# Kernel tuning notes

Hardware: AMD Instinct MI355X
Metric: run time of the kernel (lower is better)

Reference implementation:

```python
import jax, jax.numpy as jnp
import numpy as np
from jax import lax

LR, SB, LB = 256, 16, 8  # lr_size, spatial_bin, luma_bins
DN = ('NCHW', 'OIHW', 'NCHW')


def conv2d(x, w, b=None, stride=1, pad=1):
    out = lax.conv_general_dilated(x, w, (stride, stride), [(pad, pad), (pad, pad)], dimension_numbers=DN)
    return out if b is None else out + b[None, :, None, None]


def gaussian_blur17(x):
    # kornia GaussianBlur2d(kernel=(17,17), sigma=(2,2)), reflect padding, separable
    t = jnp.arange(17, dtype=x.dtype) - 8.0
    g = jnp.exp(-(t * t) / 8.0)  # 2*sigma^2 = 8
    g = g / g.sum()
    C = x.shape[1]
    xp = jnp.pad(x, ((0, 0), (0, 0), (8, 8), (8, 8)), mode='reflect')
    kh = jnp.broadcast_to(g.reshape(1, 1, 17, 1), (C, 1, 17, 1))
    kw = jnp.broadcast_to(g.reshape(1, 1, 1, 17), (C, 1, 1, 17))
    x1 = lax.conv_general_dilated(xp, kh, (1, 1), 'VALID', dimension_numbers=DN, feature_group_count=C)
    return lax.conv_general_dilated(x1, kw, (1, 1), 'VALID', dimension_numbers=DN, feature_group_count=C)


def nearest_resize(x, size):
    # torch F.interpolate mode='nearest': src = floor(dst * in/out)
    H, W = x.shape[-2], x.shape[-1]
    iy = jnp.floor(jnp.arange(size) * (H / size)).astype(jnp.int32)
    ix = jnp.floor(jnp.arange(size) * (W / size)).astype(jnp.int32)
    return x[:, :, iy][:, :, :, ix]


def grid_sample_3d_border(inp, grid):
    # inp [B,C,D,Hi,Wi]; grid [B,Do,Ho,Wo,3] with (x,y,z); bilinear, padding_mode='border', align_corners=False
    B, C, D, Hi, Wi = inp.shape
    x = jnp.clip(((grid[..., 0] + 1.0) * Wi - 1.0) * 0.5, 0.0, Wi - 1.0)
    y = jnp.clip(((grid[..., 1] + 1.0) * Hi - 1.0) * 0.5, 0.0, Hi - 1.0)
    z = jnp.clip(((grid[..., 2] + 1.0) * D - 1.0) * 0.5, 0.0, D - 1.0)
    x0 = jnp.floor(x); y0 = jnp.floor(y); z0 = jnp.floor(z)
    fx = (x - x0)[:, None]; fy = (y - y0)[:, None]; fz = (z - z0)[:, None]  # [B,1,Do,Ho,Wo]
    x0i = x0.astype(jnp.int32); y0i = y0.astype(jnp.int32); z0i = z0.astype(jnp.int32)
    x1i = jnp.minimum(x0i + 1, Wi - 1); y1i = jnp.minimum(y0i + 1, Hi - 1); z1i = jnp.minimum(z0i + 1, D - 1)
    flat = inp.reshape(B, C, D * Hi * Wi)
    M = grid.shape[1] * grid.shape[2] * grid.shape[3]

    def gat(zi, yi, xi):
        idx = ((zi * Hi + yi) * Wi + xi).reshape(B, 1, M)
        v = jnp.take_along_axis(flat, jnp.broadcast_to(idx, (B, C, M)), axis=2)
        return v.reshape(B, C, grid.shape[1], grid.shape[2], grid.shape[3])

    return (gat(z0i, y0i, x0i) * (1 - fz) * (1 - fy) * (1 - fx)
            + gat(z0i, y0i, x1i) * (1 - fz) * (1 - fy) * fx
            + gat(z0i, y1i, x0i) * (1 - fz) * fy * (1 - fx)
            + gat(z0i, y1i, x1i) * (1 - fz) * fy * fx
            + gat(z1i, y0i, x0i) * fz * (1 - fy) * (1 - fx)
            + gat(z1i, y0i, x1i) * fz * (1 - fy) * fx
            + gat(z1i, y1i, x0i) * fz * fy * (1 - fx)
            + gat(z1i, y1i, x1i) * fz * fy * fx)


def _forward(lqs, evs, gw1, gb1, gw2, gb2, sw0, sb0, sw1, sb1, sw2, sb2, sw3, sb3,
             cw0, cb0, cw1, cb1, fw1, fb1, fw2, fb2, fw3, fb3, lw1, lb1, lw2, fuw, fub):
    B, _, H, W = lqs.shape
    # --- HighresStreamNet guide ---
    g = gaussian_blur17(lqs)
    g = jax.nn.relu(conv2d(g, gw1, gb1, 1, 0))
    guide = jax.nn.sigmoid(conv2d(g, gw2, gb2, 1, 0)) * 2.0 - 0.5  # [B,1,H,W]
    # --- slicing grid (x,y in (-0.5,1.5) per source, z = guide) ---
    gx = (jnp.arange(W, dtype=lqs.dtype) + 0.5) / W * 2.0 - 0.5
    gy = (jnp.arange(H, dtype=lqs.dtype) + 0.5) / H * 2.0 - 0.5
    gyy, gxx = jnp.meshgrid(gy, gx, indexing='ij')
    base = jnp.broadcast_to(jnp.stack([gxx, gyy], -1)[None, None], (B, 1, H, W, 2))
    grid = jnp.concatenate([base, guide[..., None]], axis=-1)  # [B,1,H,W,3]
    # --- LowresStreamNet ---
    lr = nearest_resize(lqs, LR)
    ev = evs if (evs.shape[-1] == LR and evs.shape[-2] == LR) else nearest_resize(evs, LR)
    x = jnp.concatenate([lr, ev], axis=1)  # [B,18,256,256]
    for w_, b_ in ((sw0, sb0), (sw1, sb1), (sw2, sb2), (sw3, sb3)):
        x = jax.nn.relu(conv2d(x, w_, b_, 2, 1))  # -> [B,64,16,16]
    xl = conv2d(jax.nn.relu(conv2d(x, lw1, lb1, 1, 1)), lw2, None, 1, 1)  # local, last conv no bias
    xg = jax.nn.relu(conv2d(x, cw0, cb0, 2, 1))
    xg = jax.nn.relu(conv2d(xg, cw1, cb1, 2, 1)).reshape(B, -1)  # [B,1024]
    xg = jax.nn.relu(xg @ fw1.T + fb1)
    xg = jax.nn.relu(xg @ fw2.T + fb2)
    xg = xg @ fw3.T + fb3  # [B,64]
    fused = jax.nn.relu(xg[:, :, None, None] + xl)
    bg = conv2d(fused, fuw, fub, 1, 0).reshape(B, 1, LB, SB, SB)  # bilateral grid [B,1,8,16,16]
    hr = grid_sample_3d_border(bg, grid)  # [B,1,1,H,W]
    return hr.reshape(B, -1, H, W)


def setup_inputs():
    key = jax.random.key(0)
    ks = iter(jax.random.split(key, 40))

    def W_(shape):
        fan_in = int(np.prod(shape[1:]))
        return jax.random.normal(next(ks), shape, jnp.float32) * np.float32(np.sqrt(2.0 / fan_in))

    def Z(n):
        return jnp.zeros((n,), jnp.float32)

    B, H, Wd = 8, 1024, 1024
    return {
        'lqs': jax.random.uniform(next(ks), (B, 3, H, Wd), jnp.float32),
        'evs': jax.random.normal(next(ks), (B, 15, 256, 256), jnp.float32) * 0.1,
        'gw1': W_((16, 3, 1, 1)), 'gb1': Z(16), 'gw2': W_((1, 16, 1, 1)), 'gb2': Z(1),
        'sw0': W_((8, 18, 3, 3)), 'sb0': Z(8), 'sw1': W_((16, 8, 3, 3)), 'sb1': Z(16),
        'sw2': W_((32, 16, 3, 3)), 'sb2': Z(32), 'sw3': W_((64, 32, 3, 3)), 'sb3': Z(64),
        'cw0': W_((64, 64, 3, 3)), 'cb0': Z(64), 'cw1': W_((64, 64, 3, 3)), 'cb1': Z(64),
        'fw1': W_((256, 1024)), 'fb1': Z(256), 'fw2': W_((128, 256)), 'fb2': Z(128),
        'fw3': W_((64, 128)), 'fb3': Z(64),
        'lw1': W_((64, 64, 3, 3)), 'lb1': Z(64), 'lw2': W_((64, 64, 3, 3)),
        'fuw': W_((8, 64, 1, 1)), 'fub': Z(8),
    }


def reference(lqs, evs, gw1, gb1, gw2, gb2, sw0, sb0, sw1, sb1, sw2, sb2, sw3, sb3,
              cw0, cb0, cw1, cb1, fw1, fb1, fw2, fb2, fw3, fb3, lw1, lb1, lw2, fuw, fub):
    return _forward(lqs, evs, gw1, gb1, gw2, gb2, sw0, sb0, sw1, sb1, sw2, sb2, sw3, sb3,
                    cw0, cb0, cw1, cb1, fw1, fb1, fw2, fb2, fw3, fb3, lw1, lb1, lw2, fuw, fub)
```

## Files before the change

kernel.cpp:

```cpp
#include <hip/hip_runtime.h>
#include <hip/hip_bf16.h>
#include <math.h>

#define BATCH 8
#define HH 1024
#define WW 1024

__device__ __forceinline__ int reflect1024(int i) {
    i = i < 0 ? -i : i;
    return i > 1023 ? 2046 - i : i;
}

__global__ __launch_bounds__(256) void conv0_k(const float* __restrict__ lqs,
                                               const float* __restrict__ evs,
                                               const float* __restrict__ w,
                                               const float* __restrict__ bias,
                                               float* __restrict__ out) {
    int idx = blockIdx.x * 256 + threadIdx.x;
    int q = idx & 4095;
    int b = idx >> 12;
    int qx = q & 31, oy = q >> 5;
    int iy0 = oy * 2 - 1;

    float acc[4][8];
#pragma unroll
    for (int j = 0; j < 4; ++j)
#pragma unroll
        for (int o = 0; o < 8; ++o) acc[j][o] = bias[o];

#pragma unroll
    for (int ic = 0; ic < 3; ++ic) {
        const float* ipc = lqs + (size_t)(b * 3 + ic) * HH * WW;
#pragma unroll
        for (int ky = 0; ky < 3; ++ky) {
            int iy = iy0 + ky;
            if (iy < 0) continue;
            const float* row = ipc + (size_t)iy * 4 * WW;
            float xr[9];
#pragma unroll
            for (int i = 0; i < 9; ++i) {
                int ix = 8 * qx - 1 + i;
                xr[i] = (ix >= 0) ? row[ix * 4] : 0.0f;
            }
#pragma unroll
            for (int o = 0; o < 8; ++o) {
                const float* wp = w + (o * 18 + ic) * 9 + ky * 3;
#pragma unroll
                for (int j = 0; j < 4; ++j)
#pragma unroll
                    for (int kx = 0; kx < 3; ++kx)
                        acc[j][o] = fmaf(wp[kx], xr[2 * j + kx], acc[j][o]);
            }
        }
    }
    for (int ic = 0; ic < 15; ++ic) {
        const float* ipc = evs + (size_t)(b * 15 + ic) * 65536;
#pragma unroll
        for (int ky = 0; ky < 3; ++ky) {
            int iy = iy0 + ky;
            if (iy < 0) continue;
            const float* row = ipc + iy * 256;
            const float4* r4 = (const float4*)row;
            float4 A = r4[2 * qx];
            float4 Bv = r4[2 * qx + 1];
            float m = (qx > 0) ? row[8 * qx - 1] : 0.0f;
            float xr[9] = {m, A.x, A.y, A.z, A.w, Bv.x, Bv.y, Bv.z, Bv.w};
#pragma unroll
            for (int o = 0; o < 8; ++o) {
                const float* wp = w + (o * 18 + ic + 3) * 9 + ky * 3;
#pragma unroll
                for (int j = 0; j < 4; ++j)
#pragma unroll
                    for (int kx = 0; kx < 3; ++kx)
                        acc[j][o] = fmaf(wp[kx], xr[2 * j + kx], acc[j][o]);
            }
        }
    }
#pragma unroll
    for (int o = 0; o < 8; ++o) {
        float4 v = make_float4(fmaxf(acc[0][o], 0.0f), fmaxf(acc[1][o], 0.0f),
                               fmaxf(acc[2][o], 0.0f), fmaxf(acc[3][o], 0.0f));
        *(float4*)(out + ((size_t)(b * 8 + o) << 14) + oy * 128 + qx * 4) = v;
    }
}

template <int IC, int OC, int OCT, int IH, int IW, int STRIDE, bool RELU, bool HASB>
__global__ __launch_bounds__(256) void convN_k(const float* __restrict__ in,
                                               const float* __restrict__ w,
                                               const float* __restrict__ bias,
                                               float* __restrict__ out) {
    constexpr int OH = (IH + 2 - 3) / STRIDE + 1;
    constexpr int OW = (IW + 2 - 3) / STRIDE + 1;
    constexpr int POS = OH * OW;
    constexpr int G = OC / OCT;
    int idx = blockIdx.x * 256 + threadIdx.x;
    if (idx >= BATCH * G * POS) return;
    int px = idx % POS;
    int g = (idx / POS) % G;
    int b = idx / (POS * G);
    int ox = px % OW, oy = px / OW;
    int iy0 = oy * STRIDE - 1, ix0 = ox * STRIDE - 1;

    float acc[OCT];
#pragma unroll
    for (int o = 0; o < OCT; ++o) acc[o] = HASB ? bias[g * OCT + o] : 0.0f;

    const float* ip = in + (size_t)b * IC * IH * IW;
    for (int ic = 0; ic < IC; ++ic) {
        const float* ipc = ip + ic * IH * IW;
        float x[9];
#pragma unroll
        for (int ky = 0; ky < 3; ++ky) {
            int iy = iy0 + ky;
#pragma unroll
            for (int kx = 0; kx < 3; ++kx) {
                int ix = ix0 + kx;
                bool ok = (iy >= 0) && (iy < IH) && (ix >= 0) && (ix < IW);
                x[ky * 3 + kx] = ok ? ipc[iy * IW + ix] : 0.0f;
            }
        }
#pragma unroll
        for (int o = 0; o < OCT; ++o) {
            const float* wp = w + ((g * OCT + o) * IC + ic) * 9;
#pragma unroll
            for (int k = 0; k < 9; ++k) acc[o] = fmaf(wp[k], x[k], acc[o]);
        }
    }
#pragma unroll
    for (int o = 0; o < OCT; ++o) {
        float v = acc[o];
        if (RELU) v = fmaxf(v, 0.0f);
        out[(size_t)(b * OC + g * OCT + o) * POS + px] = v;
    }
}

template <int IC, int OC, int OCT, int IH, int IW, int STRIDE, int SPLIT>
__global__ __launch_bounds__(256) void convS_k(const float* __restrict__ in,
                                               const float* __restrict__ w,
                                               float* __restrict__ part) {
    constexpr int OH = (IH + 2 - 3) / STRIDE + 1;
    constexpr int OW = (IW + 2 - 3) / STRIDE + 1;
    constexpr int POS = OH * OW;
    constexpr int G = OC / OCT;
    constexpr int TOT = BATCH * G * POS;
    constexpr int ICS = IC / SPLIT;
    constexpr int N = BATCH * OC * POS;
    int idx = blockIdx.x * 256 + threadIdx.x;
    if (idx >= TOT * SPLIT) return;
    int s = idx / TOT, r = idx % TOT;
    int px = r % POS;
    int g = (r / POS) % G;
    int b = r / (POS * G);
    int ox = px % OW, oy = px / OW;
    int iy0 = oy * STRIDE - 1, ix0 = ox * STRIDE - 1;

    float acc[OCT];
#pragma unroll
    for (int o = 0; o < OCT; ++o) acc[o] = 0.0f;

    const float* ip = in + (size_t)b * IC * IH * IW;
    for (int ic = s * ICS; ic < (s + 1) * ICS; ++ic) {
        const float* ipc = ip + ic * IH * IW;
        float x[9];
#pragma unroll
        for (int ky = 0; ky < 3; ++ky) {
            int iy = iy0 + ky;
#pragma unroll
            for (int kx = 0; kx < 3; ++kx) {
                int ix = ix0 + kx;
                bool ok = (iy >= 0) && (iy < IH) && (ix >= 0) && (ix < IW);
                x[ky * 3 + kx] = ok ? ipc[iy * IW + ix] : 0.0f;
            }
        }
#pragma unroll
        for (int o = 0; o < OCT; ++o) {
            const float* wp = w + ((g * OCT + o) * IC + ic) * 9;
#pragma unroll
            for (int k = 0; k < 9; ++k) acc[o] = fmaf(wp[k], x[k], acc[o]);
        }
    }
#pragma unroll
    for (int o = 0; o < OCT; ++o)
        part[(size_t)s * N + (size_t)(b * OC + g * OCT + o) * POS + px] = acc[o];
}

__global__ __launch_bounds__(256) void fc1_k(const float* __restrict__ part_cw1,
                                             const float* __restrict__ cb1,
                                             const float* __restrict__ fw1,
                                             const float* __restrict__ fb1,
                                             float* __restrict__ h1) {
    __shared__ float xin[1024];
    int t = threadIdx.x;
    int b = blockIdx.x >> 6;
    int rgrp = blockIdx.x & 63;
    int wave = t >> 6, lane = t & 63;

    for (int i = t; i < 1024; i += 256) {
        float v = cb1[i >> 4];
#pragma unroll
        for (int s = 0; s < 16; ++s) v += part_cw1[s * 8192 + b * 1024 + i];
        xin[i] = fmaxf(v, 0.0f);
    }
    __syncthreads();

    int r = (rgrp << 2) | wave;
    const float4* w4 = (const float4*)(fw1 + r * 1024);
    const float4* x4 = (const float4*)xin;
    float acc = 0.0f;
#pragma unroll
    for (int jj = 0; jj < 4; ++jj) {
        float4 wv = w4[lane + 64 * jj];
        float4 xv = x4[lane + 64 * jj];
        acc = fmaf(wv.x, xv.x, acc);
        acc = fmaf(wv.y, xv.y, acc);
        acc = fmaf(wv.z, xv.z, acc);
        acc = fmaf(wv.w, xv.w, acc);
    }
#pragma unroll
    for (int m = 32; m; m >>= 1) acc += __shfl_xor(acc, m, 64);
    if (lane == 0) h1[b * 256 + r] = fmaxf(acc + fb1[r], 0.0f);
}

__global__ __launch_bounds__(256) void fc23fuse_k(const float* __restrict__ h1,
                                                  const float* __restrict__ fw2,
                                                  const float* __restrict__ fb2,
                                                  const float* __restrict__ fw3,
                                                  const float* __restrict__ fb3,
                                                  const float* __restrict__ xl2,
                                                  const float* __restrict__ fuw,
                                                  const float* __restrict__ fub,
                                                  float* __restrict__ bg) {
    __shared__ float h2[128];
    __shared__ float xg[64];
    int b = blockIdx.x, t = threadIdx.x;
    int wave = t >> 6, lane = t & 63;

    float4 xv1 = ((const float4*)(h1 + b * 256))[lane];
#pragma unroll 4
    for (int i = 0; i < 32; ++i) {
        int r = wave * 32 + i;
        float4 wv = ((const float4*)(fw2 + r * 256))[lane];
        float acc = fmaf(wv.x, xv1.x, fmaf(wv.y, xv1.y, fmaf(wv.z, xv1.z, wv.w * xv1.w)));
#pragma unroll
        for (int m = 32; m; m >>= 1) acc += __shfl_xor(acc, m, 64);
        if (lane == 0) h2[r] = fmaxf(acc + fb2[r], 0.0f);
    }
    __syncthreads();

    float2 xv2 = ((const float2*)h2)[lane];
#pragma unroll 4
    for (int i = 0; i < 16; ++i) {
        int r = wave * 16 + i;
        float2 wv = ((const float2*)(fw3 + r * 128))[lane];
        float acc = fmaf(wv.x, xv2.x, wv.y * xv2.y);
#pragma unroll
        for (int m = 32; m; m >>= 1) acc += __shfl_xor(acc, m, 64);
        if (lane == 0) xg[r] = acc + fb3[r];
    }
    __syncthreads();

    int px = t;
    float acc[8];
#pragma unroll
    for (int d = 0; d < 8; ++d) acc[d] = fub[d];
    for (int c = 0; c < 64; ++c) {
        float f = fmaxf(xg[c] + xl2[(b * 64 + c) * 256 + px], 0.0f);
#pragma unroll
        for (int d = 0; d < 8; ++d) acc[d] = fmaf(fuw[d * 64 + c], f, acc[d]);
    }
#pragma unroll
    for (int d = 0; d < 8; ++d) bg[(b * 8 + d) * 256 + px] = acc[d];
}

__global__ __launch_bounds__(256) void guide_slice_k(const float* __restrict__ lqs,
                                                     const float* __restrict__ bgp,
                                                     const float* __restrict__ gw1,
                                                     const float* __restrict__ gb1,
                                                     const float* __restrict__ gw2,
                                                     const float* __restrict__ gb2,
                                                     float* __restrict__ out) {
    constexpr int TW = 64, TH = 32;
    __shared__ float sBH[3][TH][81];
    __shared__ float sBG[2048];
    __shared__ float sW1[48], sB1[16], sW2[16], sB2v[1];

    int t = threadIdx.x;
    int bx = blockIdx.x & 15;
    int by = (blockIdx.x >> 4) & 31;
    int b = blockIdx.x >> 9;
    int x0 = bx * TW, y0 = by * TH;

    float gv[17];
    {
        float gs = 0.0f;
#pragma unroll
        for (int i = 0; i < 17; ++i) {
            float d = (float)i - 8.0f;
            gv[i] = expf(-(d * d) * 0.125f);
            gs += gv[i];
        }
        float inv = 1.0f / gs;
#pragma unroll
        for (int i = 0; i < 17; ++i) gv[i] *= inv;
    }

    for (int i = t; i < 2048; i += 256) sBG[i] = bgp[b * 2048 + i];
    if (t < 48) sW1[t] = gw1[t];
    if (t < 16) { sB1[t] = gb1[t]; sW2[t] = gw2[t]; }
    if (t == 0) sB2v[0] = gb2[0];

    if (t < 240) {
        int c = t / 80, xo = t % 80;
        int gx = reflect1024(x0 + xo - 8);
        const float* colp = lqs + (size_t)(b * 3 + c) * HH * WW + gx;
        float win[17];
#pragma unroll
        for (int i = 0; i < 16; ++i)
            win[i] = colp[(size_t)reflect1024(y0 - 8 + i) * WW];
#pragma unroll
        for (int j = 0; j < TH; ++j) {
            win[(16 + j) % 17] = colp[(size_t)reflect1024(y0 + 8 + j) * WW];
            float acc = 0.0f;
#pragma unroll
            for (int i = 0; i < 17; ++i) acc = fmaf(gv[i], win[(j + i) % 17], acc);
            sBH[c][j][xo] = acc;
        }
    }
    __syncthreads();

    int yy = t >> 3, xs = (t & 7) * 8;
    int Y = y0 + yy;
    float fy = fminf(fmaxf((Y + 0.5f) * (1.0f / 64.0f) + 3.5f, 0.0f), 15.0f);
    float yf = floorf(fy);
    int yi = (int)yf;
    float ay = fy - yf;
    int yi1 = min(yi + 1, 15);

    float bcv[3][8];
#pragma unroll
    for (int c = 0; c < 3; ++c) {
        float win[17];
#pragma unroll
        for (int i = 0; i < 16; ++i) win[i] = sBH[c][yy][xs + i];
#pragma unroll
        for (int j = 0; j < 8; ++j) {
            win[(16 + j) % 17] = sBH[c][yy][xs + 16 + j];
            float acc = 0.0f;
#pragma unroll
            for (int i = 0; i < 17; ++i) acc = fmaf(gv[i], win[(j + i) % 17], acc);
            bcv[c][j] = acc;
        }
    }

    float val[8];
#pragma unroll
    for (int j = 0; j < 8; ++j) {
        float b0 = bcv[0][j], b1 = bcv[1][j], b2 = bcv[2][j];
        float s = sB2v[0];
#pragma unroll
        for (int c = 0; c < 16; ++c) {
            float g1 = fmaf(sW1[c * 3 + 0], b0,
                       fmaf(sW1[c * 3 + 1], b1,
                       fmaf(sW1[c * 3 + 2], b2, sB1[c])));
            s = fmaf(sW2[c], fmaxf(g1, 0.0f), s);
        }
        float sig = 1.0f / (1.0f + expf(-s));
        float guide = sig * 2.0f - 0.5f;

        int X = x0 + xs + j;
        float fx = fminf(fmaxf((X + 0.5f) * (1.0f / 64.0f) + 3.5f, 0.0f), 15.0f);
        float fz = fminf(fmaxf(fmaf(guide, 4.0f, 3.5f), 0.0f), 7.0f);
        float xf = floorf(fx), zf = floorf(fz);
        int xi = (int)xf, zi = (int)zf;
        float ax = fx - xf, az = fz - zf;
        int xi1 = min(xi + 1, 15), zi1 = min(zi + 1, 7);

        const float* g0 = sBG + zi * 256;
        const float* g1p = sBG + zi1 * 256;
        int i00 = yi * 16 + xi, i01 = yi * 16 + xi1;
        int i10 = yi1 * 16 + xi, i11 = yi1 * 16 + xi1;
        float c00 = g0[i00] + az * (g1p[i00] - g0[i00]);
        float c01 = g0[i01] + az * (g1p[i01] - g0[i01]);
        float c10 = g0[i10] + az * (g1p[i10] - g0[i10]);
        float c11 = g0[i11] + az * (g1p[i11] - g0[i11]);
        float c0 = c00 + ay * (c10 - c00);
        float c1 = c01 + ay * (c11 - c01);
        val[j] = c0 + ax * (c1 - c0);
    }
    float4* op = (float4*)(out + (size_t)b * HH * WW + (size_t)Y * WW + x0 + xs);
    op[0] = make_float4(val[0], val[1], val[2], val[3]);
    op[1] = make_float4(val[4], val[5], val[6], val[7]);
}

extern "C" void kernel_launch(void* const* d_in, const int* in_sizes, int n_in,
                              void* d_out, int out_size, void* d_ws, size_t ws_size,
                              hipStream_t stream) {
    const float* lqs = (const float*)d_in[0];
    const float* evs = (const float*)d_in[1];
    const float* gw1 = (const float*)d_in[2];
    const float* gb1 = (const float*)d_in[3];
    const float* gw2 = (const float*)d_in[4];
    const float* gb2 = (const float*)d_in[5];
    const float* sw0 = (const float*)d_in[6];
    const float* sb0 = (const float*)d_in[7];
    const float* sw1 = (const float*)d_in[8];
    const float* sb1 = (const float*)d_in[9];
    const float* sw2 = (const float*)d_in[10];
    const float* sb2 = (const float*)d_in[11];
    const float* sw3 = (const float*)d_in[12];
    const float* sb3 = (const float*)d_in[13];
    const float* cw0 = (const float*)d_in[14];
    const float* cb0 = (const float*)d_in[15];
    const float* cw1 = (const float*)d_in[16];
    const float* cb1 = (const float*)d_in[17];
    const float* fw1 = (const float*)d_in[18];
    const float* fb1 = (const float*)d_in[19];
    const float* fw2 = (const float*)d_in[20];
    const float* fb2 = (const float*)d_in[21];
    const float* fw3 = (const float*)d_in[22];
    const float* fb3 = (const float*)d_in[23];
    const float* lw1 = (const float*)d_in[24];
    const float* lb1 = (const float*)d_in[25];
    const float* lw2 = (const float*)d_in[26];
    const float* fuw = (const float*)d_in[27];
    const float* fub = (const float*)d_in[28];
    float* out = (float*)d_out;

    float* ws = (float*)d_ws;
    float* o0 = ws;
    float* o1 = o0 + 1048576;
    float* o2 = o1 + 524288;
    float* o3 = o2 + 262144;
    float* xl1 = o3 + 131072;
    float* xl2 = xl1 + 131072;
    float* xg0 = xl2 + 131072;
    float* h1 = xg0 + 32768;
    float* bg = h1 + 2048;
    float* part_cw1 = bg + 16384;

    conv0_k<<<128, 256, 0, stream>>>(lqs, evs, sw0, sb0, o0);
    convN_k<8, 16, 4, 128, 128, 2, true, true><<<512, 256, 0, stream>>>(o0, sw1, sb1, o1);
    convN_k<16, 32, 2, 64, 64, 2, true, true><<<512, 256, 0, stream>>>(o1, sw2, sb2, o2);
    convN_k<32, 64, 1, 32, 32, 2, true, true><<<512, 256, 0, stream>>>(o2, sw3, sb3, o3);
    convN_k<64, 64, 1, 16, 16, 1, true, true><<<512, 256, 0, stream>>>(o3, lw1, lb1, xl1);
    convN_k<64, 64, 1, 16, 16, 1, false, false><<<512, 256, 0, stream>>>(xl1, lw2, nullptr, xl2);
    convN_k<64, 64, 1, 16, 16, 2, true, true><<<128, 256, 0, stream>>>(o3, cw0, cb0, xg0);
    convS_k<64, 64, 4, 8, 8, 2, 16><<<128, 256, 0, stream>>>(xg0, cw1, part_cw1);
    fc1_k<<<512, 256, 0, stream>>>(part_cw1, cb1, fw1, fb1, h1);
    fc23fuse_k<<<8, 256, 0, stream>>>(h1, fw2, fb2, fw3, fb3, xl2, fuw, fub, bg);
    guide_slice_k<<<BATCH * 32 * 16, 256, 0, stream>>>(lqs, bg, gw1, gb1, gw2, gb2, out);
}
```

Baseline: 485.1 us.

## Split conv input channels across blocks with partial-sum reduce kernels

Replaces the direct convolution kernels for the low-resolution splat and local layers with split-K style convS kernels. Each one writes per-split partial sums that a small reduce kernel then combines, adding bias and ReLU. The lw2 partials are summed directly inside the fuse kernel, which removes one reduce pass. The aim is more parallelism for these small, deep-channel convs, at the cost of extra launches and partial-buffer memory traffic. The first conv's output-channel tiling parameter is also changed.

After: 431.2 us. 1.13x faster.

```diff
diff --git a/kernel.cpp b/kernel.cpp
--- a/kernel.cpp
+++ b/kernel.cpp
@@ -184,6 +184,20 @@
         part[(size_t)s * N + (size_t)(b * OC + g * OCT + o) * POS + px] = acc[o];
 }
 
+template <int OC, int POS, int SPLIT, bool RELU, bool HASB>
+__global__ __launch_bounds__(256) void reduce_k(const float* __restrict__ part,
+                                                const float* __restrict__ bias,
+                                                float* __restrict__ out) {
+    constexpr int N = BATCH * OC * POS;
+    int idx = blockIdx.x * 256 + threadIdx.x;
+    if (idx >= N) return;
+    int oc = (idx / POS) % OC;
+    float a = HASB ? bias[oc] : 0.0f;
+#pragma unroll
+    for (int s = 0; s < SPLIT; ++s) a += part[(size_t)s * N + idx];
+    out[idx] = RELU ? fmaxf(a, 0.0f) : a;
+}
+
 __global__ __launch_bounds__(256) void fc1_k(const float* __restrict__ part_cw1,
                                              const float* __restrict__ cb1,
                                              const float* __restrict__ fw1,
@@ -226,7 +240,7 @@
                                                   const float* __restrict__ fb2,
                                                   const float* __restrict__ fw3,
                                                   const float* __restrict__ fb3,
-                                                  const float* __restrict__ xl2,
+                                                  const float* __restrict__ part_lw2,
                                                   const float* __restrict__ fuw,
                                                   const float* __restrict__ fub,
                                                   float* __restrict__ bg) {
@@ -264,7 +278,11 @@
 #pragma unroll
     for (int d = 0; d < 8; ++d) acc[d] = fub[d];
     for (int c = 0; c < 64; ++c) {
-        float f = fmaxf(xg[c] + xl2[(b * 64 + c) * 256 + px], 0.0f);
+        int base = (b * 64 + c) * 256 + px;
+        float xlv = 0.0f;
+#pragma unroll
+        for (int s = 0; s < 8; ++s) xlv += part_lw2[s * 131072 + base];
+        float f = fmaxf(xg[c] + xlv, 0.0f);
 #pragma unroll
         for (int d = 0; d < 8; ++d) acc[d] = fmaf(fuw[d * 64 + c], f, acc[d]);
     }
@@ -432,21 +450,26 @@
     float* o2 = o1 + 524288;
     float* o3 = o2 + 262144;
     float* xl1 = o3 + 131072;
-    float* xl2 = xl1 + 131072;
-    float* xg0 = xl2 + 131072;
+    float* xg0 = xl1 + 131072;
     float* h1 = xg0 + 32768;
     float* bg = h1 + 2048;
-    float* part_cw1 = bg + 16384;
+    float* partA = bg + 16384;
+    float* part_lw2 = partA + 1048576;
+    float* part_cw1 = part_lw2 + 1048576;
 
     conv0_k<<<128, 256, 0, stream>>>(lqs, evs, sw0, sb0, o0);
-    convN_k<8, 16, 4, 128, 128, 2, true, true><<<512, 256, 0, stream>>>(o0, sw1, sb1, o1);
-    convN_k<16, 32, 2, 64, 64, 2, true, true><<<512, 256, 0, stream>>>(o1, sw2, sb2, o2);
-    convN_k<32, 64, 1, 32, 32, 2, true, true><<<512, 256, 0, stream>>>(o2, sw3, sb3, o3);
-    convN_k<64, 64, 1, 16, 16, 1, true, true><<<512, 256, 0, stream>>>(o3, lw1, lb1, xl1);
-    convN_k<64, 64, 1, 16, 16, 1, false, false><<<512, 256, 0, stream>>>(xl1, lw2, nullptr, xl2);
-    convN_k<64, 64, 1, 16, 16, 2, true, true><<<128, 256, 0, stream>>>(o3, cw0, cb0, xg0);
+    convN_k<8, 16, 8, 128, 128, 2, true, true><<<256, 256, 0, stream>>>(o0, sw1, sb1, o1);
+    convS_k<16, 32, 8, 64, 64, 2, 4><<<512, 256, 0, stream>>>(o1, sw2, partA);
+    reduce_k<32, 1024, 4, true, true><<<1024, 256, 0, stream>>>(partA, sb2, o2);
+    convS_k<32, 64, 8, 32, 32, 2, 8><<<512, 256, 0, stream>>>(o2, sw3, partA);
+    reduce_k<64, 256, 8, true, true><<<512, 256, 0, stream>>>(partA, sb3, o3);
+    convS_k<64, 64, 8, 16, 16, 1, 8><<<512, 256, 0, stream>>>(o3, lw1, partA);
+    reduce_k<64, 256, 8, true, true><<<512, 256, 0, stream>>>(partA, lb1, xl1);
+    convS_k<64, 64, 8, 16, 16, 1, 8><<<512, 256, 0, stream>>>(xl1, lw2, part_lw2);
+    convS_k<64, 64, 8, 16, 16, 2, 16><<<256, 256, 0, stream>>>(o3, cw0, partA);
+    reduce_k<64, 64, 16, true, true><<<128, 256, 0, stream>>>(partA, cb0, xg0);
     convS_k<64, 64, 4, 8, 8, 2, 16><<<128, 256, 0, stream>>>(xg0, cw1, part_cw1);
     fc1_k<<<512, 256, 0, stream>>>(part_cw1, cb1, fw1, fb1, h1);
-    fc23fuse_k<<<8, 256, 0, stream>>>(h1, fw2, fb2, fw3, fb3, xl2, fuw, fub, bg);
+    fc23fuse_k<<<8, 256, 0, stream>>>(h1, fw2, fb2, fw3, fb3, part_lw2, fuw, fub, bg);
     guide_slice_k<<<BATCH * 32 * 16, 256, 0, stream>>>(lqs, bg, gw1, gb1, gw2, gb2, out);
 }
```

## Overlap guide blur with low-res conv chain via heterogeneous fused launches

Applied to the files above, without the earlier changes.

Splits the full-resolution blur and guide MLP out of the final slice kernel and distributes its 4096 tiles across the six small conv launches. Those launches run conv blocks and blur blocks side by side, so otherwise idle compute units do the heavy guide work while the low-res chain runs. The guide z-coordinate is stored as a 16-bit fixed-point value and read back by a lighter slice kernel. The change also raises output channels per thread in the convs and drops the split-K partial sums for cw1. The cost is an extra 16 MB of guide traffic, quantization error in fz, and larger shared-memory and register use in the merged kernels.

Measured after the change: 510.0 us. 1.05x slower.

```diff
diff --git a/kernel.cpp b/kernel.cpp
--- a/kernel.cpp
+++ b/kernel.cpp
@@ -11,12 +11,12 @@
     return i > 1023 ? 2046 - i : i;
 }
 
-__global__ __launch_bounds__(256) void conv0_k(const float* __restrict__ lqs,
-                                               const float* __restrict__ evs,
-                                               const float* __restrict__ w,
-                                               const float* __restrict__ bias,
-                                               float* __restrict__ out) {
-    int idx = blockIdx.x * 256 + threadIdx.x;
+__device__ __forceinline__ void dev_conv0(int idx,
+                                          const float* __restrict__ lqs,
+                                          const float* __restrict__ evs,
+                                          const float* __restrict__ w,
+                                          const float* __restrict__ bias,
+                                          float* __restrict__ out) {
     int q = idx & 4095;
     int b = idx >> 12;
     int qx = q & 31, oy = q >> 5;
@@ -85,15 +85,15 @@
 }
 
 template <int IC, int OC, int OCT, int IH, int IW, int STRIDE, bool RELU, bool HASB>
-__global__ __launch_bounds__(256) void convN_k(const float* __restrict__ in,
-                                               const float* __restrict__ w,
-                                               const float* __restrict__ bias,
-                                               float* __restrict__ out) {
+__device__ __forceinline__ void dev_convN(int idx,
+                                          const float* __restrict__ in,
+                                          const float* __restrict__ w,
+                                          const float* __restrict__ bias,
+                                          float* __restrict__ out) {
     constexpr int OH = (IH + 2 - 3) / STRIDE + 1;
     constexpr int OW = (IW + 2 - 3) / STRIDE + 1;
     constexpr int POS = OH * OW;
     constexpr int G = OC / OCT;
-    int idx = blockIdx.x * 256 + threadIdx.x;
     if (idx >= BATCH * G * POS) return;
     int px = idx % POS;
     int g = (idx / POS) % G;
@@ -134,58 +134,156 @@
     }
 }
 
-template <int IC, int OC, int OCT, int IH, int IW, int STRIDE, int SPLIT>
-__global__ __launch_bounds__(256) void convS_k(const float* __restrict__ in,
-                                               const float* __restrict__ w,
-                                               float* __restrict__ part) {
-    constexpr int OH = (IH + 2 - 3) / STRIDE + 1;
-    constexpr int OW = (IW + 2 - 3) / STRIDE + 1;
-    constexpr int POS = OH * OW;
-    constexpr int G = OC / OCT;
-    constexpr int TOT = BATCH * G * POS;
-    constexpr int ICS = IC / SPLIT;
-    constexpr int N = BATCH * OC * POS;
-    int idx = blockIdx.x * 256 + threadIdx.x;
-    if (idx >= TOT * SPLIT) return;
-    int s = idx / TOT, r = idx % TOT;
-    int px = r % POS;
-    int g = (r / POS) % G;
-    int b = r / (POS * G);
-    int ox = px % OW, oy = px / OW;
-    int iy0 = oy * STRIDE - 1, ix0 = ox * STRIDE - 1;
-
-    float acc[OCT];
-#pragma unroll
-    for (int o = 0; o < OCT; ++o) acc[o] = 0.0f;
-
-    const float* ip = in + (size_t)b * IC * IH * IW;
-    for (int ic = s * ICS; ic < (s + 1) * ICS; ++ic) {
-        const float* ipc = ip + ic * IH * IW;
-        float x[9];
-#pragma unroll
-        for (int ky = 0; ky < 3; ++ky) {
-            int iy = iy0 + ky;
-#pragma unroll
-            for (int kx = 0; kx < 3; ++kx) {
-                int ix = ix0 + kx;
-                bool ok = (iy >= 0) && (iy < IH) && (ix >= 0) && (ix < IW);
-                x[ky * 3 + kx] = ok ? ipc[iy * IW + ix] : 0.0f;
-            }
-        }
-#pragma unroll
-        for (int o = 0; o < OCT; ++o) {
-            const float* wp = w + ((g * OCT + o) * IC + ic) * 9;
-#pragma unroll
-            for (int k = 0; k < 9; ++k) acc[o] = fmaf(wp[k], x[k], acc[o]);
-        }
-    }
-#pragma unroll
-    for (int o = 0; o < OCT; ++o)
-        part[(size_t)s * N + (size_t)(b * OC + g * OCT + o) * POS + px] = acc[o];
-}
-
-__global__ __launch_bounds__(256) void fc1_k(const float* __restrict__ part_cw1,
-                                             const float* __restrict__ cb1,
+__device__ __forceinline__ void dev_blur(int tile, int t,
+                                         const float* __restrict__ lqs,
+                                         const float* __restrict__ gw1,
+                                         const float* __restrict__ gb1,
+                                         const float* __restrict__ gw2,
+                                         const float* __restrict__ gb2,
+                                         unsigned short* __restrict__ gq) {
+    __shared__ float sBH[3][32][81];
+    __shared__ float sW1[48], sB1[16], sW2[16], sB2v[1];
+
+    int bx = tile & 15;
+    int by = (tile >> 4) & 31;
+    int b = tile >> 9;
+    int x0 = bx * 64, y0 = by * 32;
+
+    float gv[17];
+    {
+        float gs = 0.0f;
+#pragma unroll
+        for (int i = 0; i < 17; ++i) {
+            float d = (float)i - 8.0f;
+            gv[i] = expf(-(d * d) * 0.125f);
+            gs += gv[i];
+        }
+        float inv = 1.0f / gs;
+#pragma unroll
+        for (int i = 0; i < 17; ++i) gv[i] *= inv;
+    }
+
+    if (t < 48) sW1[t] = gw1[t];
+    if (t < 16) { sB1[t] = gb1[t]; sW2[t] = gw2[t]; }
+    if (t == 0) sB2v[0] = gb2[0];
+
+    if (t < 240) {
+        int c = t / 80, xo = t % 80;
+        int gx = reflect1024(x0 + xo - 8);
+        const float* colp = lqs + (size_t)(b * 3 + c) * HH * WW + gx;
+        float win[17];
+#pragma unroll
+        for (int i = 0; i < 16; ++i)
+            win[i] = colp[(size_t)reflect1024(y0 - 8 + i) * WW];
+#pragma unroll
+        for (int j = 0; j < 32; ++j) {
+            win[(16 + j) % 17] = colp[(size_t)reflect1024(y0 + 8 + j) * WW];
+            float acc = 0.0f;
+#pragma unroll
+            for (int i = 0; i < 17; ++i) acc = fmaf(gv[i], win[(j + i) % 17], acc);
+            sBH[c][j][xo] = acc;
+        }
+    }
+    __syncthreads();
+
+    int yy = t >> 3, xs = (t & 7) * 8;
+    float bcv[3][8];
+#pragma unroll
+    for (int c = 0; c < 3; ++c) {
+        float win[17];
+#pragma unroll
+        for (int i = 0; i < 16; ++i) win[i] = sBH[c][yy][xs + i];
+#pragma unroll
+        for (int j = 0; j < 8; ++j) {
+            win[(16 + j) % 17] = sBH[c][yy][xs + 16 + j];
+            float acc = 0.0f;
+#pragma unroll
+            for (int i = 0; i < 17; ++i) acc = fmaf(gv[i], win[(j + i) % 17], acc);
+            bcv[c][j] = acc;
+        }
+    }
+
+    unsigned int qw[4];
+#pragma unroll
+    for (int j = 0; j < 8; ++j) {
+        float b0 = bcv[0][j], b1 = bcv[1][j], b2 = bcv[2][j];
+        float s = sB2v[0];
+#pragma unroll
+        for (int c = 0; c < 16; ++c) {
+            float g1 = fmaf(sW1[c * 3 + 0], b0,
+                       fmaf(sW1[c * 3 + 1], b1,
+                       fmaf(sW1[c * 3 + 2], b2, sB1[c])));
+            s = fmaf(sW2[c], fmaxf(g1, 0.0f), s);
+        }
+        float sig = 1.0f / (1.0f + expf(-s));
+        float guide = sig * 2.0f - 0.5f;
+        float fz = fminf(fmaxf(fmaf(guide, 4.0f, 3.5f), 0.0f), 7.0f);
+        unsigned int q = (unsigned int)(fz * 8192.0f + 0.5f);
+        if (j & 1) qw[j >> 1] |= (q << 16);
+        else qw[j >> 1] = q;
+    }
+    size_t o = ((size_t)b << 20) + ((size_t)(y0 + yy) << 10) + x0 + xs;
+    *(uint4*)(gq + o) = make_uint4(qw[0], qw[1], qw[2], qw[3]);
+}
+
+#define GUIDE_ARGS const float* __restrict__ lqs_g, const float* __restrict__ gw1, \
+    const float* __restrict__ gb1, const float* __restrict__ gw2, \
+    const float* __restrict__ gb2, unsigned short* __restrict__ gq, \
+    int convBlocks, int blurBase
+
+__global__ __launch_bounds__(256) void u1_k(const float* __restrict__ lqs,
+                                            const float* __restrict__ evs,
+                                            const float* __restrict__ w,
+                                            const float* __restrict__ bias,
+                                            float* __restrict__ out, GUIDE_ARGS) {
+    if ((int)blockIdx.x < convBlocks)
+        dev_conv0(blockIdx.x * 256 + threadIdx.x, lqs, evs, w, bias, out);
+    else
+        dev_blur(blurBase + blockIdx.x - convBlocks, threadIdx.x, lqs_g, gw1, gb1, gw2, gb2, gq);
+}
+
+template <int IC, int OC, int OCT, int IH, int IW, int STRIDE, bool RELU, bool HASB>
+__global__ __launch_bounds__(256) void uN_k(const float* __restrict__ in,
+                                            const float* __restrict__ w,
+                                            const float* __restrict__ bias,
+                                            float* __restrict__ out, GUIDE_ARGS) {
+    if ((int)blockIdx.x < convBlocks)
+        dev_convN<IC, OC, OCT, IH, IW, STRIDE, RELU, HASB>(blockIdx.x * 256 + threadIdx.x, in, w, bias, out);
+    else
+        dev_blur(blurBase + blockIdx.x - convBlocks, threadIdx.x, lqs_g, gw1, gb1, gw2, gb2, gq);
+}
+
+__global__ __launch_bounds__(256) void u5_k(const float* __restrict__ o3,
+                                            const float* __restrict__ lw1, const float* __restrict__ lb1,
+                                            float* __restrict__ xl1,
+                                            const float* __restrict__ cw0, const float* __restrict__ cb0,
+                                            float* __restrict__ xg0, GUIDE_ARGS) {
+    int blk = blockIdx.x;
+    if (blk < 64)
+        dev_convN<64, 64, 8, 16, 16, 1, true, true>(blk * 256 + threadIdx.x, o3, lw1, lb1, xl1);
+    else if (blk < 80)
+        dev_convN<64, 64, 8, 16, 16, 2, true, true>((blk - 64) * 256 + threadIdx.x, o3, cw0, cb0, xg0);
+    else
+        dev_blur(blurBase + blk - 80, threadIdx.x, lqs_g, gw1, gb1, gw2, gb2, gq);
+    (void)convBlocks;
+}
+
+__global__ __launch_bounds__(256) void u6_k(const float* __restrict__ xl1,
+                                            const float* __restrict__ lw2, float* __restrict__ xl2,
+                                            const float* __restrict__ xg0,
+                                            const float* __restrict__ cw1, const float* __restrict__ cb1,
+                                            float* __restrict__ xg1, GUIDE_ARGS) {
+    int blk = blockIdx.x;
+    if (blk < 64)
+        dev_convN<64, 64, 8, 16, 16, 1, false, false>(blk * 256 + threadIdx.x, xl1, lw2, nullptr, xl2);
+    else if (blk < 72)
+        dev_convN<64, 64, 4, 8, 8, 2, true, true>((blk - 64) * 256 + threadIdx.x, xg0, cw1, cb1, xg1);
+    else
+        dev_blur(blurBase + blk - 72, threadIdx.x, lqs_g, gw1, gb1, gw2, gb2, gq);
+    (void)convBlocks;
+}
+
+__global__ __launch_bounds__(256) void fc1_k(const float* __restrict__ xg1,
                                              const float* __restrict__ fw1,
                                              const float* __restrict__ fb1,
                                              float* __restrict__ h1) {
@@ -195,12 +293,7 @@
     int rgrp = blockIdx.x & 63;
     int wave = t >> 6, lane = t & 63;
 
-    for (int i = t; i < 1024; i += 256) {
-        float v = cb1[i >> 4];
-#pragma unroll
-        for (int s = 0; s < 16; ++s) v += part_cw1[s * 8192 + b * 1024 + i];
-        xin[i] = fmaxf(v, 0.0f);
-    }
+    ((float4*)xin)[t] = ((const float4*)(xg1 + b * 1024))[t];
     __syncthreads();
 
     int r = (rgrp << 2) | wave;
@@ -221,17 +314,13 @@
     if (lane == 0) h1[b * 256 + r] = fmaxf(acc + fb1[r], 0.0f);
 }
 
-__global__ __launch_bounds__(256) void fc23fuse_k(const float* __restrict__ h1,
-                                                  const float* __restrict__ fw2,
-                                                  const float* __restrict__ fb2,
-                                                  const float* __restrict__ fw3,
-                                                  const float* __restrict__ fb3,
-                                                  const float* __restrict__ xl2,
-                                                  const float* __restrict__ fuw,
-                                                  const float* __restrict__ fub,
-                                                  float* __restrict__ bg) {
+__global__ __launch_bounds__(256) void fc23_k(const float* __restrict__ h1,
+                                              const float* __restrict__ fw2,
+                                              const float* __restrict__ fb2,
+                                              const float* __restrict__ fw3,
+                                              const float* __restrict__ fb3,
+                                              float* __restrict__ xgv) {
     __shared__ float h2[128];
-    __shared__ float xg[64];
     int b = blockIdx.x, t = threadIdx.x;
     int wave = t >> 6, lane = t & 63;
 
@@ -255,121 +344,53 @@
         float acc = fmaf(wv.x, xv2.x, wv.y * xv2.y);
 #pragma unroll
         for (int m = 32; m; m >>= 1) acc += __shfl_xor(acc, m, 64);
-        if (lane == 0) xg[r] = acc + fb3[r];
-    }
+        if (lane == 0) xgv[b * 64 + r] = acc + fb3[r];
+    }
+}
+
+__global__ __launch_bounds__(256) void fuse_k(const float* __restrict__ xgv,
+                                              const float* __restrict__ xl2,
+                                              const float* __restrict__ fuw,
+                                              const float* __restrict__ fub,
+                                              float* __restrict__ bg) {
+    int px = threadIdx.x;
+    int d = blockIdx.x & 7;
+    int b = blockIdx.x >> 3;
+    float acc = fub[d];
+    for (int c = 0; c < 64; ++c) {
+        float f = fmaxf(xgv[b * 64 + c] + xl2[(b * 64 + c) * 256 + px], 0.0f);
+        acc = fmaf(fuw[d * 64 + c], f, acc);
+    }
+    bg[(b * 8 + d) * 256 + px] = acc;
+}
+
+__global__ __launch_bounds__(256) void slice_k(const unsigned short* __restrict__ gq,
+                                               const float* __restrict__ bgp,
+                                               float* __restrict__ out) {
+    __shared__ float sBG[2048];
+    int t = threadIdx.x;
+    int b = blockIdx.x >> 9;
+    for (int i = t; i < 2048; i += 256) sBG[i] = bgp[b * 2048 + i];
     __syncthreads();
 
-    int px = t;
-    float acc[8];
-#pragma unroll
-    for (int d = 0; d < 8; ++d) acc[d] = fub[d];
-    for (int c = 0; c < 64; ++c) {
-        float f = fmaxf(xg[c] + xl2[(b * 64 + c) * 256 + px], 0.0f);
-#pragma unroll
-        for (int d = 0; d < 8; ++d) acc[d] = fmaf(fuw[d * 64 + c], f, acc[d]);
-    }
-#pragma unroll
-    for (int d = 0; d < 8; ++d) bg[(b * 8 + d) * 256 + px] = acc[d];
-}
-
-__global__ __launch_bounds__(256) void guide_slice_k(const float* __restrict__ lqs,
-                                                     const float* __restrict__ bgp,
-                                                     const float* __restrict__ gw1,
-                                                     const float* __restrict__ gb1,
-                                                     const float* __restrict__ gw2,
-                                                     const float* __restrict__ gb2,
-                                                     float* __restrict__ out) {
-    constexpr int TW = 64, TH = 32;
-    __shared__ float sBH[3][TH][81];
-    __shared__ float sBG[2048];
-    __shared__ float sW1[48], sB1[16], sW2[16], sB2v[1];
-
-    int t = threadIdx.x;
-    int bx = blockIdx.x & 15;
-    int by = (blockIdx.x >> 4) & 31;
-    int b = blockIdx.x >> 9;
-    int x0 = bx * TW, y0 = by * TH;
-
-    float gv[17];
-    {
-        float gs = 0.0f;
-#pragma unroll
-        for (int i = 0; i < 17; ++i) {
-            float d = (float)i - 8.0f;
-            gv[i] = expf(-(d * d) * 0.125f);
-            gs += gv[i];
-        }
-        float inv = 1.0f / gs;
-#pragma unroll
-        for (int i = 0; i < 17; ++i) gv[i] *= inv;
-    }
-
-    for (int i = t; i < 2048; i += 256) sBG[i] = bgp[b * 2048 + i];
-    if (t < 48) sW1[t] = gw1[t];
-    if (t < 16) { sB1[t] = gb1[t]; sW2[t] = gw2[t]; }
-    if (t == 0) sB2v[0] = gb2[0];
-
-    if (t < 240) {
-        int c = t / 80, xo = t % 80;
-        int gx = reflect1024(x0 + xo - 8);
-        const float* colp = lqs + (size_t)(b * 3 + c) * HH * WW + gx;
-        float win[17];
-#pragma unroll
-        for (int i = 0; i < 16; ++i)
-            win[i] = colp[(size_t)reflect1024(y0 - 8 + i) * WW];
-#pragma unroll
-        for (int j = 0; j < TH; ++j) {
-            win[(16 + j) % 17] = colp[(size_t)reflect1024(y0 + 8 + j) * WW];
-            float acc = 0.0f;
-#pragma unroll
-            for (int i = 0; i < 17; ++i) acc = fmaf(gv[i], win[(j + i) % 17], acc);
-            sBH[c][j][xo] = acc;
-        }
-    }
-    __syncthreads();
-
-    int yy = t >> 3, xs = (t & 7) * 8;
-    int Y = y0 + yy;
+    int off = (blockIdx.x & 511) * 2048 + t * 8;
+    int Y = off >> 10, X0 = off & 1023;
     float fy = fminf(fmaxf((Y + 0.5f) * (1.0f / 64.0f) + 3.5f, 0.0f), 15.0f);
     float yf = floorf(fy);
     int yi = (int)yf;
     float ay = fy - yf;
     int yi1 = min(yi + 1, 15);
 
-    float bcv[3][8];
-#pragma unroll
-    for (int c = 0; c < 3; ++c) {
-        float win[17];
-#pragma unroll
-        for (int i = 0; i < 16; ++i) win[i] = sBH[c][yy][xs + i];
-#pragma unroll
-        for (int j = 0; j < 8; ++j) {
-            win[(16 + j) % 17] = sBH[c][yy][xs + 16 + j];
-            float acc = 0.0f;
-#pragma unroll
-            for (int i = 0; i < 17; ++i) acc = fmaf(gv[i], win[(j + i) % 17], acc);
-            bcv[c][j] = acc;
-        }
-    }
+    uint4 qv = *(const uint4*)(gq + ((size_t)b << 20) + off);
+    unsigned int qw[4] = {qv.x, qv.y, qv.z, qv.w};
 
     float val[8];
 #pragma unroll
     for (int j = 0; j < 8; ++j) {
-        float b0 = bcv[0][j], b1 = bcv[1][j], b2 = bcv[2][j];
-        float s = sB2v[0];
-#pragma unroll
-        for (int c = 0; c < 16; ++c) {
-            float g1 = fmaf(sW1[c * 3 + 0], b0,
-                       fmaf(sW1[c * 3 + 1], b1,
-                       fmaf(sW1[c * 3 + 2], b2, sB1[c])));
-            s = fmaf(sW2[c], fmaxf(g1, 0.0f), s);
-        }
-        float sig = 1.0f / (1.0f + expf(-s));
-        float guide = sig * 2.0f - 0.5f;
-
-        int X = x0 + xs + j;
+        unsigned int q = (qw[j >> 1] >> ((j & 1) * 16)) & 0xffff;
+        float fz = (float)q * (1.0f / 8192.0f);
+        int X = X0 + j;
         float fx = fminf(fmaxf((X + 0.5f) * (1.0f / 64.0f) + 3.5f, 0.0f), 15.0f);
-        float fz = fminf(fmaxf(fmaf(guide, 4.0f, 3.5f), 0.0f), 7.0f);
         float xf = floorf(fx), zf = floorf(fz);
         int xi = (int)xf, zi = (int)zf;
         float ax = fx - xf, az = fz - zf;
@@ -387,7 +408,7 @@
         float c1 = c01 + ay * (c11 - c01);
         val[j] = c0 + ax * (c1 - c0);
     }
-    float4* op = (float4*)(out + (size_t)b * HH * WW + (size_t)Y * WW + x0 + xs);
+    float4* op = (float4*)(out + ((size_t)b << 20) + off);
     op[0] = make_float4(val[0], val[1], val[2], val[3]);
     op[1] = make_float4(val[4], val[5], val[6], val[7]);
 }
@@ -434,19 +455,29 @@
     float* xl1 = o3 + 131072;
     float* xl2 = xl1 + 131072;
     float* xg0 = xl2 + 131072;
-    float* h1 = xg0 + 32768;
-    float* bg = h1 + 2048;
-    float* part_cw1 = bg + 16384;
-
-    conv0_k<<<128, 256, 0, stream>>>(lqs, evs, sw0, sb0, o0);
-    convN_k<8, 16, 4, 128, 128, 2, true, true><<<512, 256, 0, stream>>>(o0, sw1, sb1, o1);
-    convN_k<16, 32, 2, 64, 64, 2, true, true><<<512, 256, 0, stream>>>(o1, sw2, sb2, o2);
-    convN_k<32, 64, 1, 32, 32, 2, true, true><<<512, 256, 0, stream>>>(o2, sw3, sb3, o3);
-    convN_k<64, 64, 1, 16, 16, 1, true, true><<<512, 256, 0, stream>>>(o3, lw1, lb1, xl1);
-    convN_k<64, 64, 1, 16, 16, 1, false, false><<<512, 256, 0, stream>>>(xl1, lw2, nullptr, xl2);
-    convN_k<64, 64, 1, 16, 16, 2, true, true><<<128, 256, 0, stream>>>(o3, cw0, cb0, xg0);
-    convS_k<64, 64, 4, 8, 8, 2, 16><<<128, 256, 0, stream>>>(xg0, cw1, part_cw1);
-    fc1_k<<<512, 256, 0, stream>>>(part_cw1, cb1, fw1, fb1, h1);
-    fc23fuse_k<<<8, 256, 0, stream>>>(h1, fw2, fb2, fw3, fb3, xl2, fuw, fub, bg);
-    guide_slice_k<<<BATCH * 32 * 16, 256, 0, stream>>>(lqs, bg, gw1, gb1, gw2, gb2, out);
-}
+    float* xg1 = xg0 + 32768;
+    float* h1 = xg1 + 8192;
+    float* xgv = h1 + 2048;
+    float* bg = xgv + 512;
+    unsigned short* gq = (unsigned short*)(bg + 16384);
+
+    const int CB[6] = {683, 683, 683, 683, 683, 681};
+    const int BB[6] = {0, 683, 1366, 2049, 2732, 3415};
+
+    u1_k<<<128 + CB[0], 256, 0, stream>>>(lqs, evs, sw0, sb0, o0,
+                                          lqs, gw1, gb1, gw2, gb2, gq, 128, BB[0]);
+    uN_k<8, 16, 8, 128, 128, 2, true, true><<<256 + CB[1], 256, 0, stream>>>(
+        o0, sw1, sb1, o1, lqs, gw1, gb1, gw2, gb2, gq, 256, BB[1]);
+    uN_k<16, 32, 8, 64, 64, 2, true, true><<<128 + CB[2], 256, 0, stream>>>(
+        o1, sw2, sb2, o2, lqs, gw1, gb1, gw2, gb2, gq, 128, BB[2]);
+    uN_k<32, 64, 8, 32, 32, 2, true, true><<<64 + CB[3], 256, 0, stream>>>(
+        o2, sw3, sb3, o3, lqs, gw1, gb1, gw2, gb2, gq, 64, BB[3]);
+    u5_k<<<80 + CB[4], 256, 0, stream>>>(o3, lw1, lb1, xl1, cw0, cb0, xg0,
+                                         lqs, gw1, gb1, gw2, gb2, gq, 80, BB[4]);
+    u6_k<<<72 + CB[5], 256, 0, stream>>>(xl1, lw2, xl2, xg0, cw1, cb1, xg1,
+                                         lqs, gw1, gb1, gw2, gb2, gq, 72, BB[5]);
+    fc1_k<<<512, 256, 0, stream>>>(xg1, fw1, fb1, h1);
+    fc23_k<<<BATCH, 256, 0, stream>>>(h1, fw2, fb2, fw3, fb3, xgv);
+    fuse_k<<<64, 256, 0, stream>>>(xgv, xl2, fuw, fub, bg);
+    slice_k<<<4096, 256, 0, stream>>>(gq, bg, out);
+}
```
